# Performance work log

Hardware: AMD Instinct MI355X
Metric: run time of the kernel (lower is better)

The kernel has to match this reference:

```python
import jax, jax.numpy as jnp
import numpy as np

DIM_IN = 1024
DIM_OUT = 1024


def setup_inputs() -> dict:
    key = jax.random.key(0)
    k1, k2, k3, k4 = jax.random.split(key, 4)
    X = jax.random.normal(k1, (4, 2048, DIM_IN), dtype=jnp.float32)
    s = 1.0 / np.sqrt(DIM_IN)
    Wq = jax.random.normal(k2, (DIM_IN, DIM_OUT), dtype=jnp.float32) * s
    Wk = jax.random.normal(k3, (DIM_IN, DIM_OUT), dtype=jnp.float32) * s
    Wv = jax.random.normal(k4, (DIM_IN, DIM_OUT), dtype=jnp.float32) * s
    return {"X": X, "Wq": Wq, "Wk": Wk, "Wv": Wv}


def reference(X, Wq, Wk, Wv):
    # X: [B, T, Din]; projections (qkv_bias=False)
    q = jnp.einsum('btd,de->bte', X, Wq)   # [B, T, Dout]
    k = jnp.einsum('btd,de->bte', X, Wk)
    v = jnp.einsum('btd,de->bte', X, Wv)
    T = X.shape[1]
    scores = jnp.einsum('bqe,bke->bqk', q, k)  # [B, T, T]
    causal = jnp.tril(jnp.ones((T, T), dtype=bool))  # mask upper triangle (future)
    scores = jnp.where(causal, scores, -jnp.inf)
    # scale=True: divide by sqrt(d); -inf stays -inf so order vs mask is irrelevant
    scores = scores / jnp.sqrt(jnp.asarray(k.shape[-1], dtype=scores.dtype))
    weights = jax.nn.softmax(scores, axis=-1)
    # dropout p=0.0 -> identity
    return jnp.einsum('bqk,bke->bqe', weights, v)
```

## Files before the change

kernel.cpp:

```cpp
#include <hip/hip_runtime.h>
#include <hip/hip_bf16.h>

typedef unsigned short u16;
typedef __bf16 bf16x8 __attribute__((ext_vector_type(8)));
typedef float f32x4 __attribute__((ext_vector_type(4)));
typedef unsigned short u16x8 __attribute__((ext_vector_type(8)));
typedef unsigned short u16x4 __attribute__((ext_vector_type(4)));

__device__ __forceinline__ float bf2f(u16 u) {
  unsigned int x = ((unsigned int)u) << 16;
  return __builtin_bit_cast(float, x);
}
__device__ __forceinline__ u16 f2bf(float f) {
  unsigned int x = __builtin_bit_cast(unsigned int, f);
  x = x + 0x7FFFu + ((x >> 16) & 1u);
  return (u16)(x >> 16);
}

__device__ __forceinline__ void gload_lds16(const u16* g, u16* l) {
  __builtin_amdgcn_global_load_lds(
      (const __attribute__((address_space(1))) unsigned int*)(unsigned long long)(uintptr_t)g,
      (__attribute__((address_space(3))) unsigned int*)(unsigned int)(uintptr_t)l,
      16, 0, 0);
}

__global__ __launch_bounds__(256) void cast_x_kernel(const float* __restrict__ X,
                                                     u16* __restrict__ Xb, long n) {
  long i = ((long)blockIdx.x * 256 + threadIdx.x) * 8;
  if (i >= n) return;
  float4 a = *reinterpret_cast<const float4*>(X + i);
  float4 b = *reinterpret_cast<const float4*>(X + i + 4);
  u16x8 o;
  o[0] = f2bf(a.x); o[1] = f2bf(a.y); o[2] = f2bf(a.z); o[3] = f2bf(a.w);
  o[4] = f2bf(b.x); o[5] = f2bf(b.y); o[6] = f2bf(b.z); o[7] = f2bf(b.w);
  *reinterpret_cast<u16x8*>(Xb + i) = o;
}

__global__ __launch_bounds__(256) void transpose_cast_w3(const float* __restrict__ Wq,
                                                         const float* __restrict__ Wk,
                                                         const float* __restrict__ Wv,
                                                         u16* __restrict__ Wt) {
  __shared__ u16 t[64][72];
  const int z = blockIdx.z;
  const float* W = (z == 0) ? Wq : (z == 1) ? Wk : Wv;
  const float scale = (z == 0) ? (1.0f / 32.0f) : 1.0f;
  u16* out = Wt + (long)z * 1048576;
  const int r0 = blockIdx.y * 64;
  const int c0 = blockIdx.x * 64;
  const int tid = threadIdx.x;
#pragma unroll
  for (int i = 0; i < 4; ++i) {
    int slot = tid + 256 * i;
    int lr = slot >> 4;
    int lc4 = slot & 15;
    float4 v = *reinterpret_cast<const float4*>(W + (long)(r0 + lr) * 1024 + c0 + lc4 * 4);
    t[lr][lc4 * 4 + 0] = f2bf(v.x * scale);
    t[lr][lc4 * 4 + 1] = f2bf(v.y * scale);
    t[lr][lc4 * 4 + 2] = f2bf(v.z * scale);
    t[lr][lc4 * 4 + 3] = f2bf(v.w * scale);
  }
  __syncthreads();
#pragma unroll
  for (int i = 0; i < 2; ++i) {
    int slot = tid + 256 * i;
    int orow = slot >> 3;
    int oc = slot & 7;
    u16x8 o;
#pragma unroll
    for (int j = 0; j < 8; ++j) o[j] = t[oc * 8 + j][orow];
    *reinterpret_cast<u16x8*>(out + (long)(c0 + orow) * 1024 + r0 + oc * 8) = o;
  }
}

template <int MODE>
__global__ __launch_bounds__(256, 2) void gemm_nt(const u16* __restrict__ Ag,
                                                  const u16* __restrict__ Bg,
                                                  void* __restrict__ Cg,
                                                  float* __restrict__ Sums,
                                                  int K, long sA, long sB, long sC) {
  int bm, bn, bz;
  if constexpr (MODE == 0) {
    const int id = blockIdx.x;
    const int xcd = id & 7, j = id >> 3;
    const int cx = xcd & 1, cy = xcd >> 1;
    bn = cx * 12 + j % 12;
    bm = cy * 16 + j / 12;
    bz = 0;
  } else if constexpr (MODE == 1) {
    const int id = blockIdx.y * 16 + blockIdx.x;
    const int xcd = id & 7, j = id >> 3;
    bn = j & 15;
    bm = (j >> 4) ? (15 - xcd) : xcd;
    bz = blockIdx.z;
    if (bn > bm) return;
  } else {
    const int id = blockIdx.y * 8 + blockIdx.x;
    const int xcd = id & 7, j = id >> 3;
    bn = j & 7;
    bm = (j >> 3) ? (15 - xcd) : xcd;
    bz = blockIdx.z;
  }

  const u16* A = Ag + (long)bz * sA;
  const u16* B = Bg + (long)bz * sB;
  const int m0 = bm * 128, n0 = bn * 128;
  int kEnd = K;
  if constexpr (MODE == 2) kEnd = m0 + 128;

  __shared__ u16 ldsA[2][8192];
  __shared__ u16 ldsB[2][8192];

  const int tid = threadIdx.x;
  const int lane = tid & 63;
  const int wid = tid >> 6;
  const int wm = wid >> 1, wn = wid & 1;
  const int l16 = lane & 15, lh = lane >> 4;
  const int srow = lane >> 3;
  const int scol = ((lane & 7) ^ srow) * 8;
  const int rsw = l16 & 7;

  bool vblk = false;
  if constexpr (MODE == 0) vblk = ((bn >> 3) == 2);

  f32x4 acc[4][4];
#pragma unroll
  for (int mi = 0; mi < 4; ++mi)
#pragma unroll
    for (int ni = 0; ni < 4; ++ni) acc[mi][ni] = (f32x4)(0.0f);

  auto stage = [&](int d, int k0) {
#pragma unroll
    for (int s = 0; s < 4; ++s) {
      const int seg = wid * 4 + s;
      const int row = seg * 8 + srow;
      gload_lds16(A + (long)(m0 + row) * K + k0 + scol, &ldsA[d][seg * 512]);
      gload_lds16(B + (long)(n0 + row) * K + k0 + scol, &ldsB[d][seg * 512]);
    }
  };

  stage(0, 0);
  int cur = 0;
  for (int k0 = 0; k0 < kEnd; k0 += 64) {
    __syncthreads();
    if (k0 + 64 < kEnd) stage(cur ^ 1, k0 + 64);
#pragma unroll
    for (int kk = 0; kk < 2; ++kk) {
      bf16x8 af[4], bfr[4];
#pragma unroll
      for (int mi = 0; mi < 4; ++mi)
        af[mi] = *reinterpret_cast<const bf16x8*>(
            &ldsA[cur][(wm * 64 + mi * 16 + l16) * 64 + (((kk * 4 + lh) ^ rsw)) * 8]);
#pragma unroll
      for (int ni = 0; ni < 4; ++ni)
        bfr[ni] = *reinterpret_cast<const bf16x8*>(
            &ldsB[cur][(wn * 64 + ni * 16 + l16) * 64 + (((kk * 4 + lh) ^ rsw)) * 8]);
      if (!vblk) {
#pragma unroll
        for (int mi = 0; mi < 4; ++mi)
#pragma unroll
          for (int ni = 0; ni < 4; ++ni)
            acc[mi][ni] = __builtin_amdgcn_mfma_f32_16x16x32_bf16(bfr[ni], af[mi], acc[mi][ni], 0, 0, 0);
      } else {
#pragma unroll
        for (int mi = 0; mi < 4; ++mi)
#pragma unroll
          for (int ni = 0; ni < 4; ++ni)
            acc[mi][ni] = __builtin_amdgcn_mfma_f32_16x16x32_bf16(af[mi], bfr[ni], acc[mi][ni], 0, 0, 0);
      }
    }
    cur ^= 1;
  }

  if constexpr (MODE == 0) {
    const int z = bn >> 3;
    const int colbase = (bn & 7) * 128;
    if (z < 2) {
      u16* C = (u16*)Cg + (long)z * 8388608;
      const long rown = (long)(m0 + wm * 64 + l16);
      const int coln = colbase + wn * 64 + lh * 4;
#pragma unroll
      for (int mi = 0; mi < 4; ++mi)
#pragma unroll
        for (int ni = 0; ni < 4; ++ni) {
          u16x4 o;
#pragma unroll
          for (int r = 0; r < 4; ++r) o[r] = f2bf(acc[mi][ni][r]);
          *reinterpret_cast<u16x4*>(&C[(rown + mi * 16) * 1024 + coln + ni * 16]) = o;
        }
    } else {
      u16* C = (u16*)Cg + 16777216;
      const int b = m0 >> 11;
      const int t0 = (m0 & 2047) + wm * 64 + lh * 4;
      const int e0 = colbase + wn * 64 + l16;
#pragma unroll
      for (int mi = 0; mi < 4; ++mi)
#pragma unroll
        for (int ni = 0; ni < 4; ++ni) {
          u16x4 o;
#pragma unroll
          for (int r = 0; r < 4; ++r) o[r] = f2bf(acc[mi][ni][r]);
          *reinterpret_cast<u16x4*>(
              &C[(long)b * 2097152 + (long)(e0 + ni * 16) * 2048 + t0 + mi * 16]) = o;
        }
    }
  } else if constexpr (MODE == 1) {
    u16* C = (u16*)Cg + (long)bz * sC;
    float* sums = Sums + (long)bz * 2048;
    const long rown = (long)(m0 + wm * 64 + l16);
    const int coln = n0 + wn * 64 + lh * 4;
#pragma unroll
    for (int mi = 0; mi < 4; ++mi) {
      const int gr = m0 + wm * 64 + l16 + mi * 16;
      float rs = 0.0f;
#pragma unroll
      for (int ni = 0; ni < 4; ++ni) {
        u16x4 o;
#pragma unroll
        for (int r = 0; r < 4; ++r) {
          const int gc = coln + ni * 16 + r;
          const float e = (gc <= gr) ? __expf(acc[mi][ni][r]) : 0.0f;
          const u16 ub = f2bf(e);
          o[r] = ub;
          rs += bf2f(ub);
        }
        *reinterpret_cast<u16x4*>(&C[(rown + mi * 16) * 2048 + coln + ni * 16]) = o;
      }
      rs += __shfl_xor(rs, 16);
      rs += __shfl_xor(rs, 32);
      if (lh == 0) atomicAdd(&sums[gr], rs);
    }
  } else {
    float* C = (float*)Cg + (long)bz * sC;
    const float* sums = Sums + (long)bz * 2048;
    const long rown = (long)(m0 + wm * 64 + l16);
    const int coln = n0 + wn * 64 + lh * 4;
#pragma unroll
    for (int mi = 0; mi < 4; ++mi) {
      const float inv = 1.0f / sums[(int)rown + mi * 16];
#pragma unroll
      for (int ni = 0; ni < 4; ++ni) {
        f32x4 v = acc[mi][ni] * inv;
        *reinterpret_cast<f32x4*>(&C[(rown + mi * 16) * 1024 + coln + ni * 16]) = v;
      }
    }
  }
}

extern "C" void kernel_launch(void* const* d_in, const int* in_sizes, int n_in,
                              void* d_out, int out_size, void* d_ws, size_t ws_size,
                              hipStream_t stream) {
  const float* X  = (const float*)d_in[0];
  const float* Wq = (const float*)d_in[1];
  const float* Wk = (const float*)d_in[2];
  const float* Wv = (const float*)d_in[3];

  u16* Xb = (u16*)d_ws;
  u16* Wt = Xb + 8388608;
  u16* Qb = Wt + 3145728;
  u16* Kb = Qb + 8388608;
  u16* Vt = Kb + 8388608;
  u16* S  = Vt + 8388608;
  float* sums = (float*)(S + 16777216);

  hipMemsetAsync(sums, 0, 4 * 2048 * sizeof(float), stream);

  cast_x_kernel<<<4096, 256, 0, stream>>>(X, Xb, 8388608L);
  transpose_cast_w3<<<dim3(16, 16, 3), 256, 0, stream>>>(Wq, Wk, Wv, Wt);

  gemm_nt<0><<<1536, 256, 0, stream>>>(Xb, Wt, Qb, nullptr, 1024, 0L, 0L, 0L);

  gemm_nt<1><<<dim3(16, 16, 4), 256, 0, stream>>>(
      Qb, Kb, S, sums, 1024, 2097152L, 2097152L, 4194304L);

  gemm_nt<2><<<dim3(8, 16, 4), 256, 0, stream>>>(
      S, Vt, (float*)d_out, sums, 2048, 4194304L, 2097152L, 2097152L);
}
```

Measured before the change: 146.5 us.

## Fuse prep kernels and move V projection into causal QK^T launch

Merges the X cast and the weight transpose-cast into one prep kernel. The first GEMM now computes only Q and K. The V projection (written transposed) runs inside the QK^T launch as extra blocks, and the QK^T grid is compacted to only the lower-triangular tiles through a linear index decode, so no blocks launch just to exit. This cuts kernel launches and early-exit blocks and lets the V work fill idle CUs during the causal score GEMM. The cost is a serial loop to decode the triangular index and more branching in one kernel.

```diff
diff --git a/kernel.cpp b/kernel.cpp
--- a/kernel.cpp
+++ b/kernel.cpp
@@ -24,30 +24,32 @@
       16, 0, 0);
 }
 
-__global__ __launch_bounds__(256) void cast_x_kernel(const float* __restrict__ X,
-                                                     u16* __restrict__ Xb, long n) {
-  long i = ((long)blockIdx.x * 256 + threadIdx.x) * 8;
-  if (i >= n) return;
-  float4 a = *reinterpret_cast<const float4*>(X + i);
-  float4 b = *reinterpret_cast<const float4*>(X + i + 4);
-  u16x8 o;
-  o[0] = f2bf(a.x); o[1] = f2bf(a.y); o[2] = f2bf(a.z); o[3] = f2bf(a.w);
-  o[4] = f2bf(b.x); o[5] = f2bf(b.y); o[6] = f2bf(b.z); o[7] = f2bf(b.w);
-  *reinterpret_cast<u16x8*>(Xb + i) = o;
-}
-
-__global__ __launch_bounds__(256) void transpose_cast_w3(const float* __restrict__ Wq,
-                                                         const float* __restrict__ Wk,
-                                                         const float* __restrict__ Wv,
-                                                         u16* __restrict__ Wt) {
+__global__ __launch_bounds__(256) void prep_kernel(const float* __restrict__ X,
+                                                   const float* __restrict__ Wq,
+                                                   const float* __restrict__ Wk,
+                                                   const float* __restrict__ Wv,
+                                                   u16* __restrict__ Xb,
+                                                   u16* __restrict__ Wt) {
+  const int id = blockIdx.x;
+  const int tid = threadIdx.x;
+  if (id < 4096) {
+    long i = ((long)id * 256 + tid) * 8;
+    float4 a = *reinterpret_cast<const float4*>(X + i);
+    float4 b = *reinterpret_cast<const float4*>(X + i + 4);
+    u16x8 o;
+    o[0] = f2bf(a.x); o[1] = f2bf(a.y); o[2] = f2bf(a.z); o[3] = f2bf(a.w);
+    o[4] = f2bf(b.x); o[5] = f2bf(b.y); o[6] = f2bf(b.z); o[7] = f2bf(b.w);
+    *reinterpret_cast<u16x8*>(Xb + i) = o;
+    return;
+  }
   __shared__ u16 t[64][72];
-  const int z = blockIdx.z;
+  const int id2 = id - 4096;
+  const int z = id2 >> 8;
   const float* W = (z == 0) ? Wq : (z == 1) ? Wk : Wv;
   const float scale = (z == 0) ? (1.0f / 32.0f) : 1.0f;
   u16* out = Wt + (long)z * 1048576;
-  const int r0 = blockIdx.y * 64;
-  const int c0 = blockIdx.x * 64;
-  const int tid = threadIdx.x;
+  const int c0 = (id2 & 15) * 64;
+  const int r0 = ((id2 >> 4) & 15) * 64;
 #pragma unroll
   for (int i = 0; i < 4; ++i) {
     int slot = tid + 256 * i;
@@ -77,32 +79,45 @@
                                                   const u16* __restrict__ Bg,
                                                   void* __restrict__ Cg,
                                                   float* __restrict__ Sums,
+                                                  const u16* __restrict__ A2,
+                                                  const u16* __restrict__ B2,
+                                                  u16* __restrict__ C2,
                                                   int K, long sA, long sB, long sC) {
-  int bm, bn, bz;
+  int bm, bn, bz = 0;
+  bool vblk = false;
+  const u16* A;
+  const u16* B;
   if constexpr (MODE == 0) {
     const int id = blockIdx.x;
     const int xcd = id & 7, j = id >> 3;
-    const int cx = xcd & 1, cy = xcd >> 1;
-    bn = cx * 12 + j % 12;
-    bm = cy * 16 + j / 12;
-    bz = 0;
+    bn = (xcd & 1) * 8 + (j & 7);
+    bm = (xcd >> 1) * 16 + (j >> 3);
+    A = Ag; B = Bg;
   } else if constexpr (MODE == 1) {
-    const int id = blockIdx.y * 16 + blockIdx.x;
-    const int xcd = id & 7, j = id >> 3;
-    bn = j & 15;
-    bm = (j >> 4) ? (15 - xcd) : xcd;
-    bz = blockIdx.z;
-    if (bn > bm) return;
+    const int id = blockIdx.x;
+    if (id < 512) {
+      vblk = true;
+      const int xcd = id & 7, j = id >> 3;
+      bm = xcd * 8 + (j >> 3);
+      bn = j & 7;
+      A = A2; B = B2;
+    } else {
+      int t = id - 512;
+      bz = t / 136; t -= bz * 136;
+      int r = 0;
+      while ((r + 1) * (r + 2) / 2 <= t) ++r;
+      bm = r; bn = t - r * (r + 1) / 2;
+      A = Ag + (long)bz * sA; B = Bg + (long)bz * sB;
+    }
   } else {
     const int id = blockIdx.y * 8 + blockIdx.x;
     const int xcd = id & 7, j = id >> 3;
     bn = j & 7;
     bm = (j >> 3) ? (15 - xcd) : xcd;
     bz = blockIdx.z;
-  }
-
-  const u16* A = Ag + (long)bz * sA;
-  const u16* B = Bg + (long)bz * sB;
+    A = Ag + (long)bz * sA; B = Bg + (long)bz * sB;
+  }
+
   const int m0 = bm * 128, n0 = bn * 128;
   int kEnd = K;
   if constexpr (MODE == 2) kEnd = m0 + 128;
@@ -119,9 +134,6 @@
   const int scol = ((lane & 7) ^ srow) * 8;
   const int rsw = l16 & 7;
 
-  bool vblk = false;
-  if constexpr (MODE == 0) vblk = ((bn >> 3) == 2);
-
   f32x4 acc[4][4];
 #pragma unroll
   for (int mi = 0; mi < 4; ++mi)
@@ -174,10 +186,23 @@
   if constexpr (MODE == 0) {
     const int z = bn >> 3;
     const int colbase = (bn & 7) * 128;
-    if (z < 2) {
-      u16* C = (u16*)Cg + (long)z * 8388608;
-      const long rown = (long)(m0 + wm * 64 + l16);
-      const int coln = colbase + wn * 64 + lh * 4;
+    u16* C = (u16*)Cg + (long)z * 8388608;
+    const long rown = (long)(m0 + wm * 64 + l16);
+    const int coln = colbase + wn * 64 + lh * 4;
+#pragma unroll
+    for (int mi = 0; mi < 4; ++mi)
+#pragma unroll
+      for (int ni = 0; ni < 4; ++ni) {
+        u16x4 o;
+#pragma unroll
+        for (int r = 0; r < 4; ++r) o[r] = f2bf(acc[mi][ni][r]);
+        *reinterpret_cast<u16x4*>(&C[(rown + mi * 16) * 1024 + coln + ni * 16]) = o;
+      }
+  } else if constexpr (MODE == 1) {
+    if (vblk) {
+      const int b = m0 >> 11;
+      const int t0 = (m0 & 2047) + wm * 64 + lh * 4;
+      const int e0 = bn * 128 + wn * 64 + l16;
 #pragma unroll
       for (int mi = 0; mi < 4; ++mi)
 #pragma unroll
@@ -185,49 +210,35 @@
           u16x4 o;
 #pragma unroll
           for (int r = 0; r < 4; ++r) o[r] = f2bf(acc[mi][ni][r]);
-          *reinterpret_cast<u16x4*>(&C[(rown + mi * 16) * 1024 + coln + ni * 16]) = o;
+          *reinterpret_cast<u16x4*>(
+              &C2[(long)b * 2097152 + (long)(e0 + ni * 16) * 2048 + t0 + mi * 16]) = o;
         }
     } else {
-      u16* C = (u16*)Cg + 16777216;
-      const int b = m0 >> 11;
-      const int t0 = (m0 & 2047) + wm * 64 + lh * 4;
-      const int e0 = colbase + wn * 64 + l16;
-#pragma unroll
-      for (int mi = 0; mi < 4; ++mi)
+      u16* C = (u16*)Cg + (long)bz * sC;
+      float* sums = Sums + (long)bz * 2048;
+      const long rown = (long)(m0 + wm * 64 + l16);
+      const int coln = n0 + wn * 64 + lh * 4;
+#pragma unroll
+      for (int mi = 0; mi < 4; ++mi) {
+        const int gr = m0 + wm * 64 + l16 + mi * 16;
+        float rs = 0.0f;
 #pragma unroll
         for (int ni = 0; ni < 4; ++ni) {
           u16x4 o;
 #pragma unroll
-          for (int r = 0; r < 4; ++r) o[r] = f2bf(acc[mi][ni][r]);
-          *reinterpret_cast<u16x4*>(
-              &C[(long)b * 2097152 + (long)(e0 + ni * 16) * 2048 + t0 + mi * 16]) = o;
+          for (int r = 0; r < 4; ++r) {
+            const int gc = coln + ni * 16 + r;
+            const float e = (gc <= gr) ? __expf(acc[mi][ni][r]) : 0.0f;
+            const u16 ub = f2bf(e);
+            o[r] = ub;
+            rs += bf2f(ub);
+          }
+          *reinterpret_cast<u16x4*>(&C[(rown + mi * 16) * 2048 + coln + ni * 16]) = o;
         }
-    }
-  } else if constexpr (MODE == 1) {
-    u16* C = (u16*)Cg + (long)bz * sC;
-    float* sums = Sums + (long)bz * 2048;
-    const long rown = (long)(m0 + wm * 64 + l16);
-    const int coln = n0 + wn * 64 + lh * 4;
-#pragma unroll
-    for (int mi = 0; mi < 4; ++mi) {
-      const int gr = m0 + wm * 64 + l16 + mi * 16;
-      float rs = 0.0f;
-#pragma unroll
-      for (int ni = 0; ni < 4; ++ni) {
-        u16x4 o;
-#pragma unroll
-        for (int r = 0; r < 4; ++r) {
-          const int gc = coln + ni * 16 + r;
-          const float e = (gc <= gr) ? __expf(acc[mi][ni][r]) : 0.0f;
-          const u16 ub = f2bf(e);
-          o[r] = ub;
-          rs += bf2f(ub);
-        }
-        *reinterpret_cast<u16x4*>(&C[(rown + mi * 16) * 2048 + coln + ni * 16]) = o;
-      }
-      rs += __shfl_xor(rs, 16);
-      rs += __shfl_xor(rs, 32);
-      if (lh == 0) atomicAdd(&sums[gr], rs);
+        rs += __shfl_xor(rs, 16);
+        rs += __shfl_xor(rs, 32);
+        if (lh == 0) atomicAdd(&sums[gr], rs);
+      }
     }
   } else {
     float* C = (float*)Cg + (long)bz * sC;
@@ -264,14 +275,16 @@
 
   hipMemsetAsync(sums, 0, 4 * 2048 * sizeof(float), stream);
 
-  cast_x_kernel<<<4096, 256, 0, stream>>>(X, Xb, 8388608L);
-  transpose_cast_w3<<<dim3(16, 16, 3), 256, 0, stream>>>(Wq, Wk, Wv, Wt);
-
-  gemm_nt<0><<<1536, 256, 0, stream>>>(Xb, Wt, Qb, nullptr, 1024, 0L, 0L, 0L);
-
-  gemm_nt<1><<<dim3(16, 16, 4), 256, 0, stream>>>(
-      Qb, Kb, S, sums, 1024, 2097152L, 2097152L, 4194304L);
-
-  gemm_nt<2><<<dim3(8, 16, 4), 256, 0, stream>>>(
-      S, Vt, (float*)d_out, sums, 2048, 4194304L, 2097152L, 2097152L);
-}
+  prep_kernel<<<4864, 256, 0, stream>>>(X, Wq, Wk, Wv, Xb, Wt);
+
+  gemm_nt<0><<<1024, 256, 0, stream>>>(Xb, Wt, Qb, nullptr,
+                                       nullptr, nullptr, nullptr, 1024, 0L, 0L, 0L);
+
+  gemm_nt<1><<<1056, 256, 0, stream>>>(Qb, Kb, S, sums,
+                                       Xb, Wt + 2097152, Vt,
+                                       1024, 2097152L, 2097152L, 4194304L);
+
+  gemm_nt<2><<<dim3(8, 16, 4), 256, 0, stream>>>(S, Vt, (float*)d_out, sums,
+                                                 nullptr, nullptr, nullptr,
+                                                 2048, 4194304L, 2097152L, 2097152L);
+}
```

Measured after the change: 156.1 us. 1.07x slower.

## Use 8 waves per GEMM block and merge cast/transpose prep kernels

Applied to the files above, without the earlier changes.

Each GEMM block now runs 512 threads (8 waves in a 2x4 layout). Every wave computes a 64x32 sub-tile instead of 64x64, which halves the per-wave accumulator registers and gives more waves per CU to hide latency. The LDS staging is re-indexed so all 512 threads issue two direct-to-LDS loads per operand. The X cast and W transpose-cast kernels are merged into one launch to save a kernel launch. In exchange, each wave reads the A fragments again for fewer MFMAs, so LDS read traffic per MFMA goes up.

```diff
diff --git a/kernel.cpp b/kernel.cpp
--- a/kernel.cpp
+++ b/kernel.cpp
@@ -24,30 +24,32 @@
       16, 0, 0);
 }
 
-__global__ __launch_bounds__(256) void cast_x_kernel(const float* __restrict__ X,
-                                                     u16* __restrict__ Xb, long n) {
-  long i = ((long)blockIdx.x * 256 + threadIdx.x) * 8;
-  if (i >= n) return;
-  float4 a = *reinterpret_cast<const float4*>(X + i);
-  float4 b = *reinterpret_cast<const float4*>(X + i + 4);
-  u16x8 o;
-  o[0] = f2bf(a.x); o[1] = f2bf(a.y); o[2] = f2bf(a.z); o[3] = f2bf(a.w);
-  o[4] = f2bf(b.x); o[5] = f2bf(b.y); o[6] = f2bf(b.z); o[7] = f2bf(b.w);
-  *reinterpret_cast<u16x8*>(Xb + i) = o;
-}
-
-__global__ __launch_bounds__(256) void transpose_cast_w3(const float* __restrict__ Wq,
-                                                         const float* __restrict__ Wk,
-                                                         const float* __restrict__ Wv,
-                                                         u16* __restrict__ Wt) {
+__global__ __launch_bounds__(256) void prep_kernel(const float* __restrict__ X,
+                                                   const float* __restrict__ Wq,
+                                                   const float* __restrict__ Wk,
+                                                   const float* __restrict__ Wv,
+                                                   u16* __restrict__ Xb,
+                                                   u16* __restrict__ Wt) {
+  const int id = blockIdx.x;
+  const int tid = threadIdx.x;
+  if (id < 4096) {
+    long i = ((long)id * 256 + tid) * 8;
+    float4 a = *reinterpret_cast<const float4*>(X + i);
+    float4 b = *reinterpret_cast<const float4*>(X + i + 4);
+    u16x8 o;
+    o[0] = f2bf(a.x); o[1] = f2bf(a.y); o[2] = f2bf(a.z); o[3] = f2bf(a.w);
+    o[4] = f2bf(b.x); o[5] = f2bf(b.y); o[6] = f2bf(b.z); o[7] = f2bf(b.w);
+    *reinterpret_cast<u16x8*>(Xb + i) = o;
+    return;
+  }
   __shared__ u16 t[64][72];
-  const int z = blockIdx.z;
+  const int id2 = id - 4096;
+  const int z = id2 >> 8;
   const float* W = (z == 0) ? Wq : (z == 1) ? Wk : Wv;
   const float scale = (z == 0) ? (1.0f / 32.0f) : 1.0f;
   u16* out = Wt + (long)z * 1048576;
-  const int r0 = blockIdx.y * 64;
-  const int c0 = blockIdx.x * 64;
-  const int tid = threadIdx.x;
+  const int c0 = (id2 & 15) * 64;
+  const int r0 = ((id2 >> 4) & 15) * 64;
 #pragma unroll
   for (int i = 0; i < 4; ++i) {
     int slot = tid + 256 * i;
@@ -73,7 +75,7 @@
 }
 
 template <int MODE>
-__global__ __launch_bounds__(256, 2) void gemm_nt(const u16* __restrict__ Ag,
+__global__ __launch_bounds__(512, 2) void gemm_nt(const u16* __restrict__ Ag,
                                                   const u16* __restrict__ Bg,
                                                   void* __restrict__ Cg,
                                                   float* __restrict__ Sums,
@@ -113,28 +115,27 @@
   const int tid = threadIdx.x;
   const int lane = tid & 63;
   const int wid = tid >> 6;
-  const int wm = wid >> 1, wn = wid & 1;
+  const int wm = wid >> 2, wn = wid & 3;
   const int l16 = lane & 15, lh = lane >> 4;
-  const int srow = lane >> 3;
-  const int scol = ((lane & 7) ^ srow) * 8;
+  const int strow = tid >> 3;
+  const int scol = ((tid & 7) ^ (strow & 7)) * 8;
   const int rsw = l16 & 7;
 
   bool vblk = false;
   if constexpr (MODE == 0) vblk = ((bn >> 3) == 2);
 
-  f32x4 acc[4][4];
+  f32x4 acc[4][2];
 #pragma unroll
   for (int mi = 0; mi < 4; ++mi)
 #pragma unroll
-    for (int ni = 0; ni < 4; ++ni) acc[mi][ni] = (f32x4)(0.0f);
+    for (int ni = 0; ni < 2; ++ni) acc[mi][ni] = (f32x4)(0.0f);
 
   auto stage = [&](int d, int k0) {
 #pragma unroll
-    for (int s = 0; s < 4; ++s) {
-      const int seg = wid * 4 + s;
-      const int row = seg * 8 + srow;
-      gload_lds16(A + (long)(m0 + row) * K + k0 + scol, &ldsA[d][seg * 512]);
-      gload_lds16(B + (long)(n0 + row) * K + k0 + scol, &ldsB[d][seg * 512]);
+    for (int l = 0; l < 2; ++l) {
+      const int row = l * 64 + strow;
+      gload_lds16(A + (long)(m0 + row) * K + k0 + scol, &ldsA[d][l * 4096 + tid * 8]);
+      gload_lds16(B + (long)(n0 + row) * K + k0 + scol, &ldsB[d][l * 4096 + tid * 8]);
     }
   };
 
@@ -145,26 +146,26 @@
     if (k0 + 64 < kEnd) stage(cur ^ 1, k0 + 64);
 #pragma unroll
     for (int kk = 0; kk < 2; ++kk) {
-      bf16x8 af[4], bfr[4];
+      bf16x8 af[4], bfr[2];
 #pragma unroll
       for (int mi = 0; mi < 4; ++mi)
         af[mi] = *reinterpret_cast<const bf16x8*>(
             &ldsA[cur][(wm * 64 + mi * 16 + l16) * 64 + (((kk * 4 + lh) ^ rsw)) * 8]);
 #pragma unroll
-      for (int ni = 0; ni < 4; ++ni)
+      for (int ni = 0; ni < 2; ++ni)
         bfr[ni] = *reinterpret_cast<const bf16x8*>(
-            &ldsB[cur][(wn * 64 + ni * 16 + l16) * 64 + (((kk * 4 + lh) ^ rsw)) * 8]);
+            &ldsB[cur][(wn * 32 + ni * 16 + l16) * 64 + (((kk * 4 + lh) ^ rsw)) * 8]);
       if (!vblk) {
 #pragma unroll
         for (int mi = 0; mi < 4; ++mi)
 #pragma unroll
-          for (int ni = 0; ni < 4; ++ni)
+          for (int ni = 0; ni < 2; ++ni)
             acc[mi][ni] = __builtin_amdgcn_mfma_f32_16x16x32_bf16(bfr[ni], af[mi], acc[mi][ni], 0, 0, 0);
       } else {
 #pragma unroll
         for (int mi = 0; mi < 4; ++mi)
 #pragma unroll
-          for (int ni = 0; ni < 4; ++ni)
+          for (int ni = 0; ni < 2; ++ni)
             acc[mi][ni] = __builtin_amdgcn_mfma_f32_16x16x32_bf16(af[mi], bfr[ni], acc[mi][ni], 0, 0, 0);
       }
     }
@@ -177,11 +178,11 @@
     if (z < 2) {
       u16* C = (u16*)Cg + (long)z * 8388608;
       const long rown = (long)(m0 + wm * 64 + l16);
-      const int coln = colbase + wn * 64 + lh * 4;
+      const int coln = colbase + wn * 32 + lh * 4;
 #pragma unroll
       for (int mi = 0; mi < 4; ++mi)
 #pragma unroll
-        for (int ni = 0; ni < 4; ++ni) {
+        for (int ni = 0; ni < 2; ++ni) {
           u16x4 o;
 #pragma unroll
           for (int r = 0; r < 4; ++r) o[r] = f2bf(acc[mi][ni][r]);
@@ -191,11 +192,11 @@
       u16* C = (u16*)Cg + 16777216;
       const int b = m0 >> 11;
       const int t0 = (m0 & 2047) + wm * 64 + lh * 4;
-      const int e0 = colbase + wn * 64 + l16;
+      const int e0 = colbase + wn * 32 + l16;
 #pragma unroll
       for (int mi = 0; mi < 4; ++mi)
 #pragma unroll
-        for (int ni = 0; ni < 4; ++ni) {
+        for (int ni = 0; ni < 2; ++ni) {
           u16x4 o;
 #pragma unroll
           for (int r = 0; r < 4; ++r) o[r] = f2bf(acc[mi][ni][r]);
@@ -207,13 +208,13 @@
     u16* C = (u16*)Cg + (long)bz * sC;
     float* sums = Sums + (long)bz * 2048;
     const long rown = (long)(m0 + wm * 64 + l16);
-    const int coln = n0 + wn * 64 + lh * 4;
+    const int coln = n0 + wn * 32 + lh * 4;
 #pragma unroll
     for (int mi = 0; mi < 4; ++mi) {
       const int gr = m0 + wm * 64 + l16 + mi * 16;
       float rs = 0.0f;
 #pragma unroll
-      for (int ni = 0; ni < 4; ++ni) {
+      for (int ni = 0; ni < 2; ++ni) {
         u16x4 o;
 #pragma unroll
         for (int r = 0; r < 4; ++r) {
@@ -233,12 +234,12 @@
     float* C = (float*)Cg + (long)bz * sC;
     const float* sums = Sums + (long)bz * 2048;
     const long rown = (long)(m0 + wm * 64 + l16);
-    const int coln = n0 + wn * 64 + lh * 4;
+    const int coln = n0 + wn * 32 + lh * 4;
 #pragma unroll
     for (int mi = 0; mi < 4; ++mi) {
       const float inv = 1.0f / sums[(int)rown + mi * 16];
 #pragma unroll
-      for (int ni = 0; ni < 4; ++ni) {
+      for (int ni = 0; ni < 2; ++ni) {
         f32x4 v = acc[mi][ni] * inv;
         *reinterpret_cast<f32x4*>(&C[(rown + mi * 16) * 1024 + coln + ni * 16]) = v;
       }
@@ -264,14 +265,13 @@
 
   hipMemsetAsync(sums, 0, 4 * 2048 * sizeof(float), stream);
 
-  cast_x_kernel<<<4096, 256, 0, stream>>>(X, Xb, 8388608L);
-  transpose_cast_w3<<<dim3(16, 16, 3), 256, 0, stream>>>(Wq, Wk, Wv, Wt);
-
-  gemm_nt<0><<<1536, 256, 0, stream>>>(Xb, Wt, Qb, nullptr, 1024, 0L, 0L, 0L);
-
-  gemm_nt<1><<<dim3(16, 16, 4), 256, 0, stream>>>(
+  prep_kernel<<<4864, 256, 0, stream>>>(X, Wq, Wk, Wv, Xb, Wt);
+
+  gemm_nt<0><<<1536, 512, 0, stream>>>(Xb, Wt, Qb, nullptr, 1024, 0L, 0L, 0L);
+
+  gemm_nt<1><<<dim3(16, 16, 4), 512, 0, stream>>>(
       Qb, Kb, S, sums, 1024, 2097152L, 2097152L, 4194304L);
 
-  gemm_nt<2><<<dim3(8, 16, 4), 256, 0, stream>>>(
+  gemm_nt<2><<<dim3(8, 16, 4), 512, 0, stream>>>(
       S, Vt, (float*)d_out, sums, 2048, 4194304L, 2097152L, 2097152L);
 }
```

Result: no change. 145.8 us (-0.5%).
